# Optimization experiments

Measured on AMD Instinct MI355X. Metric: run time of the kernel, lower is better.

Reference implementation:

```python
import jax, jax.numpy as jnp
import numpy as np

D_MODEL = 1024
D_FF = 4096
BATCH = 4
SEQ = 2048
DECAY = 0.9
THRESH = 0.5


def setup_inputs() -> dict:
    key = jax.random.key(0)
    k1, k2, k3, k4 = jax.random.split(key, 4)
    spikes = jax.random.normal(k1, (BATCH, SEQ, D_MODEL), dtype=jnp.float32)
    # xavier-ish init scales matching gains 0.5/0.5/0.3 in the torch module
    s1 = 0.5 * np.sqrt(2.0 / (D_MODEL + D_FF))
    s2 = 0.5 * np.sqrt(2.0 / (D_MODEL + D_FF))
    sr = 0.3 * np.sqrt(2.0 / (D_MODEL + D_FF))
    W1 = jax.random.normal(k2, (D_FF, D_MODEL), dtype=jnp.float32) * s1
    W2 = jax.random.normal(k3, (D_MODEL, D_FF), dtype=jnp.float32) * s2
    Wr = jax.random.normal(k4, (D_FF, D_MODEL), dtype=jnp.float32) * sr
    return {"spikes": spikes, "W1": W1, "W2": W2, "Wr": Wr}


def reference(spikes, W1, W2, Wr):
    # spikes: [B, T, D]; W1, Wr: [F, D]; W2: [D, F]
    B, T, D = spikes.shape
    F = W1.shape[0]
    d = jnp.float32(DECAY)
    one_minus_d = jnp.float32(1.0 - DECAY)
    # Hoist time-independent projections out of the recurrence (same math as
    # the per-timestep nn.Linear calls in the torch loop).
    r_all = jax.nn.sigmoid(jnp.einsum('btd,fd->btf', spikes, Wr))  # [B,T,F]
    h_all = jnp.einsum('btd,fd->btf', spikes, W1)                   # [B,T,F]

    def step(carry, xs):
        act, rec = carry              # [B,F] each, init zeros (fresh buffers)
        r_t, h_t = xs                 # [B,F]
        rec = d * rec + one_minus_d * r_t                 # mixed receptance
        mixed = d * act + one_minus_d * h_t               # temporal state mix
        spike = (mixed > THRESH).astype(h_t.dtype)        # eval-mode spikes
        gated = spike * r_t
        # torch detaches current_activation each step
        return (jax.lax.stop_gradient(mixed), rec), gated

    init = (jnp.zeros((B, F), spikes.dtype), jnp.zeros((B, F), spikes.dtype))
    _, gated = jax.lax.scan(step,
                            init,
                            (jnp.swapaxes(r_all, 0, 1), jnp.swapaxes(h_all, 0, 1)))
    # gated: [T, B, F] -> output [B, T, D]
    out = jnp.einsum('tbf,df->btd', gated, W2)
    return out
```

## Files before the change

kernel.cpp:

```cpp
#include <hip/hip_runtime.h>
#include <math.h>

#define B_    4
#define T_    2048
#define D_    1024
#define F_    4096
#define R_    (B_*T_)
#define SEG_  64
#define L_    (T_/SEG_)
#define DECAYF 0.9f
#define OMDF   0.1f
#define FLAG_THRESH 0.45f

typedef __attribute__((ext_vector_type(4))) int   i32x4;
typedef __attribute__((ext_vector_type(8))) int   i32x8;
typedef __attribute__((ext_vector_type(4))) float f32x4;

__device__ __forceinline__ int pk_fp8x4(float x, float y, float z, float w) {
    int p = 0;
    p = __builtin_amdgcn_cvt_pk_fp8_f32(x, y, p, false);
    p = __builtin_amdgcn_cvt_pk_fp8_f32(z, w, p, true);
    return p;
}

__device__ __forceinline__ void gload_lds16(const void* g, void* l) {
    __builtin_amdgcn_global_load_lds(
        (const __attribute__((address_space(1))) unsigned int*)g,
        (__attribute__((address_space(3))) unsigned int*)l, 16, 0, 0);
}

#define KA_W1_BLOCKS  4096
#define KA_SEG_BLOCKS 256
#define KA_FLAG_BLOCKS 32

__global__ __launch_bounds__(256)
void kA_prologue(const float* __restrict__ spikes,
                 const float* __restrict__ W1,
                 unsigned char* __restrict__ w_f8,
                 float* __restrict__ seg_sum,
                 unsigned int* __restrict__ flags) {
    const int bid = blockIdx.x;
    const int tid = threadIdx.x;
    if (bid < KA_W1_BLOCKS) {
        int i = bid * 256 + tid;
        float4 v = ((const float4*)W1)[i];
        ((int*)w_f8)[i] = pk_fp8x4(8.f*v.x, 8.f*v.y, 8.f*v.z, 8.f*v.w);
    } else if (bid < KA_W1_BLOCKS + KA_SEG_BLOCKS) {
        int t = (bid - KA_W1_BLOCKS) * 256 + tid;
        int dg = t & (D_ / 4 - 1);
        int s = (t >> 8) & (SEG_ - 1);
        int b = t >> 14;
        const float4* sp4 = (const float4*)spikes;
        const int base = (b * T_ + s * L_) * (D_ / 4) + dg;
        float4 e = {0.f, 0.f, 0.f, 0.f};
#pragma unroll 8
        for (int k = 0; k < L_; ++k) {
            float4 x = sp4[base + k * (D_ / 4)];
            e.x = DECAYF * e.x + OMDF * x.x;
            e.y = DECAYF * e.y + OMDF * x.y;
            e.z = DECAYF * e.z + OMDF * x.z;
            e.w = DECAYF * e.w + OMDF * x.w;
        }
        ((float4*)seg_sum)[(b * SEG_ + s) * (D_ / 4) + dg] = e;
    } else {
        int i = (bid - KA_W1_BLOCKS - KA_SEG_BLOCKS) * 256 + tid;
        if (i < R_) flags[i] = 0u;
    }
}

__global__ __launch_bounds__(256)
void kB_seg_scan(const float* __restrict__ seg_sum,
                 float* __restrict__ start_state) {
    int g = blockIdx.x * 256 + threadIdx.x;
    int s = g & 63;
    int c = g >> 6;
    int d = c & (D_ - 1);
    int b = c >> 10;
    int idx = (b * SEG_ + s) * D_ + d;
    float v = seg_sum[idx];
    float wp = 0.0343368382f;
#pragma unroll
    for (int off = 1; off < SEG_; off <<= 1) {
        float u = __shfl_up(v, off, 64);
        if (s >= off) v += wp * u;
        wp *= wp;
    }
    float pv = __shfl_up(v, 1, 64);
    start_state[idx] = (s == 0) ? 0.f : pv;
}

__global__ __launch_bounds__(256)
void kC_ema_fp8(const float* __restrict__ spikes,
                const float* __restrict__ start_state,
                unsigned char* __restrict__ a_f8) {
    int t = blockIdx.x * 256 + threadIdx.x;
    int dg = t & (D_ / 4 - 1);
    int s = (t >> 8) & (SEG_ - 1);
    int b = t >> 14;
    const float4* sp4 = (const float4*)spikes;
    const int base = (b * T_ + s * L_) * (D_ / 4) + dg;
    float4 e = ((const float4*)start_state)[(b * SEG_ + s) * (D_ / 4) + dg];
#pragma unroll 8
    for (int k = 0; k < L_; ++k) {
        float4 x = sp4[base + k * (D_ / 4)];
        e.x = DECAYF * e.x + OMDF * x.x;
        e.y = DECAYF * e.y + OMDF * x.y;
        e.z = DECAYF * e.z + OMDF * x.z;
        e.w = DECAYF * e.w + OMDF * x.w;
        ((int*)a_f8)[base + k * (D_ / 4)] =
            pk_fp8x4(8.f*e.x, 8.f*e.y, 8.f*e.z, 8.f*e.w);
    }
}

__global__ __launch_bounds__(256)
void k2_mfma_flags(const unsigned char* __restrict__ A,
                   const unsigned char* __restrict__ Bw,
                   unsigned int* __restrict__ flags) {
    __shared__ __align__(16) unsigned char lA[128 * 128];
    __shared__ __align__(16) unsigned char lB[128 * 128];
    const int tid = threadIdx.x;
    const int w = tid >> 6;
    const int lane = tid & 63;
    const int m0 = blockIdx.y * 128;
    const int n0 = blockIdx.x * 128;
    const int wm = w >> 1, wn = w & 1;
    const int rown = lane & 15;
    const int kgrp = lane >> 4;
    const int c0 = 2 * kgrp;

    f32x4 acc[4][4] = {};

    for (int k0 = 0; k0 < D_; k0 += 128) {
        __syncthreads();
#pragma unroll
        for (int r = 0; r < 4; ++r) {
            const int Ibase = r * 256 + w * 64;
            const int I = Ibase + lane;
            const int row = I >> 3;
            const int cl = (I & 7) ^ (row & 7);
            gload_lds16(&A [(size_t)(m0 + row) * D_ + k0 + cl * 16], &lA[Ibase * 16]);
            gload_lds16(&Bw[(size_t)(n0 + row) * D_ + k0 + cl * 16], &lB[Ibase * 16]);
        }
        __syncthreads();

        i32x8 af[4], bf[4];
#pragma unroll
        for (int i = 0; i < 4; ++i) {
            const int ra = wm * 64 + i * 16 + rown;
            i32x4 lo = *(const i32x4*)&lA[ra * 128 + ((c0    ) ^ (ra & 7)) * 16];
            i32x4 hi = *(const i32x4*)&lA[ra * 128 + ((c0 + 1) ^ (ra & 7)) * 16];
            af[i] = (i32x8){lo.x, lo.y, lo.z, lo.w, hi.x, hi.y, hi.z, hi.w};
            const int rb = wn * 64 + i * 16 + rown;
            i32x4 lo2 = *(const i32x4*)&lB[rb * 128 + ((c0    ) ^ (rb & 7)) * 16];
            i32x4 hi2 = *(const i32x4*)&lB[rb * 128 + ((c0 + 1) ^ (rb & 7)) * 16];
            bf[i] = (i32x8){lo2.x, lo2.y, lo2.z, lo2.w, hi2.x, hi2.y, hi2.z, hi2.w};
        }
#pragma unroll
        for (int i = 0; i < 4; ++i)
#pragma unroll
            for (int j = 0; j < 4; ++j)
                acc[i][j] = __builtin_amdgcn_mfma_scale_f32_16x16x128_f8f6f4(
                    af[i], bf[j], acc[i][j],
                    0, 0,
                    0, 124,
                    0, 124);
    }

    const int quad = lane >> 4;
#pragma unroll
    for (int i = 0; i < 4; ++i) {
#pragma unroll
        for (int v = 0; v < 4; ++v) {
            float mx =     acc[i][0][v];
            mx = fmaxf(mx, acc[i][1][v]);
            mx = fmaxf(mx, acc[i][2][v]);
            mx = fmaxf(mx, acc[i][3][v]);
            if (mx > FLAG_THRESH)
                atomicOr(&flags[m0 + wm * 64 + i * 16 + quad * 4 + v], 1u);
        }
    }
}

__global__ __launch_bounds__(256)
void k4_output(const float* __restrict__ spikes,
               const float* __restrict__ start_state,
               const float* __restrict__ W1,
               const float* __restrict__ Wr,
               const float* __restrict__ W2,
               const unsigned int* __restrict__ flags,
               float* __restrict__ out) {
    const int row = blockIdx.x;
    const int tid = threadIdx.x;
    float4 o = {0.f, 0.f, 0.f, 0.f};

    if (flags[row] == 0u) {
        *(float4*)&out[(size_t)row * D_ + tid * 4] = o;
        return;
    }

    __shared__ float se[D_];
    __shared__ float sp[D_];
    __shared__ float red[256];
    __shared__ int nspk;
    __shared__ int spk_list[256];

    const int b = row / T_;
    const int t = row % T_;
    const int seg = t / L_;
    const int off = t % L_;
    const int segbase = (b * T_ + seg * L_) * D_;

    for (int i = tid; i < D_; i += 256) {
        float e = start_state[(b * SEG_ + seg) * D_ + i];
        for (int j = 0; j <= off; ++j)
            e = DECAYF * e + OMDF * spikes[segbase + j * D_ + i];
        se[i] = e;
        sp[i] = spikes[(size_t)row * D_ + i];
    }
    if (tid == 0) nspk = 0;
    __syncthreads();

    for (int f0 = 0; f0 < F_; f0 += 256) {
        int f = f0 + tid;
        float mix = 0.f;
        for (int k = 0; k < D_; ++k) mix += se[k] * W1[(size_t)f * D_ + k];
        if (mix > 0.5f) {
            int idx = atomicAdd(&nspk, 1);
            spk_list[idx] = f;
        }
        __syncthreads();
        int n = nspk;
        for (int i = 0; i < n; ++i) {
            int fs = spk_list[i];
            float part = 0.f;
#pragma unroll
            for (int k = 0; k < 4; ++k)
                part += sp[tid * 4 + k] * Wr[(size_t)fs * D_ + tid * 4 + k];
            red[tid] = part;
            __syncthreads();
            for (int sft = 128; sft > 0; sft >>= 1) {
                if (tid < sft) red[tid] += red[tid + sft];
                __syncthreads();
            }
            float r = 1.f / (1.f + expf(-red[0]));
            __syncthreads();
            o.x += r * W2[(size_t)(tid * 4 + 0) * F_ + fs];
            o.y += r * W2[(size_t)(tid * 4 + 1) * F_ + fs];
            o.z += r * W2[(size_t)(tid * 4 + 2) * F_ + fs];
            o.w += r * W2[(size_t)(tid * 4 + 3) * F_ + fs];
        }
        __syncthreads();
        if (tid == 0) nspk = 0;
        __syncthreads();
    }
    *(float4*)&out[(size_t)row * D_ + tid * 4] = o;
}

extern "C" void kernel_launch(void* const* d_in, const int* in_sizes, int n_in,
                              void* d_out, int out_size, void* d_ws, size_t ws_size,
                              hipStream_t stream) {
    const float* spikes = (const float*)d_in[0];
    const float* W1     = (const float*)d_in[1];
    const float* W2     = (const float*)d_in[2];
    const float* Wr     = (const float*)d_in[3];
    float* out = (float*)d_out;

    char* ws = (char*)d_ws;
    float* seg_sum      = (float*)ws;
    float* start_state  = seg_sum + (size_t)B_ * SEG_ * D_;
    unsigned int* flags = (unsigned int*)(start_state + (size_t)B_ * SEG_ * D_);
    unsigned char* a_f8 = (unsigned char*)(flags + R_);
    unsigned char* w_f8 = a_f8 + (size_t)R_ * D_;

    kA_prologue<<<KA_W1_BLOCKS + KA_SEG_BLOCKS + KA_FLAG_BLOCKS, 256, 0, stream>>>(
        spikes, W1, w_f8, seg_sum, flags);
    kB_seg_scan<<<(B_ * D_ * 64) / 256, 256, 0, stream>>>(seg_sum, start_state);
    kC_ema_fp8<<<(B_ * SEG_ * D_ / 4) / 256, 256, 0, stream>>>(spikes, start_state, a_f8);

    dim3 g2(F_ / 128, R_ / 128);
    k2_mfma_flags<<<g2, 256, 0, stream>>>(a_f8, w_f8, flags);

    k4_output<<<R_, 256, 0, stream>>>(spikes, start_state, W1, Wr, W2, flags, out);
}
```

Baseline: 203.8 us.

## Switch flag GEMM to 32x32x64 fp8 MFMA with smaller K tile

After: 379.6 us. 86.3% more time.

```diff
diff --git a/kernel.cpp b/kernel.cpp
--- a/kernel.cpp
+++ b/kernel.cpp
@@ -12,9 +12,9 @@
 #define OMDF   0.1f
 #define FLAG_THRESH 0.45f
 
-typedef __attribute__((ext_vector_type(4))) int   i32x4;
-typedef __attribute__((ext_vector_type(8))) int   i32x8;
-typedef __attribute__((ext_vector_type(4))) float f32x4;
+typedef __attribute__((ext_vector_type(4)))  int   i32x4;
+typedef __attribute__((ext_vector_type(8)))  int   i32x8;
+typedef __attribute__((ext_vector_type(16))) float f32x16;
 
 __device__ __forceinline__ int pk_fp8x4(float x, float y, float z, float w) {
     int p = 0;
@@ -112,71 +112,79 @@
     }
 }
 
-__global__ __launch_bounds__(256)
+__global__ __launch_bounds__(256, 3)
 void k2_mfma_flags(const unsigned char* __restrict__ A,
                    const unsigned char* __restrict__ Bw,
                    unsigned int* __restrict__ flags) {
-    __shared__ __align__(16) unsigned char lA[128 * 128];
-    __shared__ __align__(16) unsigned char lB[128 * 128];
+    __shared__ __align__(16) unsigned char lA[128 * 64];
+    __shared__ __align__(16) unsigned char lB[128 * 64];
     const int tid = threadIdx.x;
     const int w = tid >> 6;
     const int lane = tid & 63;
     const int m0 = blockIdx.y * 128;
     const int n0 = blockIdx.x * 128;
     const int wm = w >> 1, wn = w & 1;
-    const int rown = lane & 15;
-    const int kgrp = lane >> 4;
-    const int c0 = 2 * kgrp;
-
-    f32x4 acc[4][4] = {};
-
-    for (int k0 = 0; k0 < D_; k0 += 128) {
-        __syncthreads();
-#pragma unroll
-        for (int r = 0; r < 4; ++r) {
+    const int col = lane & 31;
+    const int kg  = lane >> 5;
+
+    int offA[2][2], offB[2][2];
+#pragma unroll
+    for (int i = 0; i < 2; ++i) {
+        const int ra = wm * 64 + i * 32 + col;
+        const int swa = (ra >> 1) & 3;
+        offA[i][0] = ra * 64 + ((2 * kg    ) ^ swa) * 16;
+        offA[i][1] = ra * 64 + ((2 * kg + 1) ^ swa) * 16;
+        const int rb = wn * 64 + i * 32 + col;
+        const int swb = (rb >> 1) & 3;
+        offB[i][0] = rb * 64 + ((2 * kg    ) ^ swb) * 16;
+        offB[i][1] = rb * 64 + ((2 * kg + 1) ^ swb) * 16;
+    }
+
+    f32x16 acc[2][2] = {};
+
+    for (int k0 = 0; k0 < D_; k0 += 64) {
+        __syncthreads();
+#pragma unroll
+        for (int r = 0; r < 2; ++r) {
             const int Ibase = r * 256 + w * 64;
             const int I = Ibase + lane;
-            const int row = I >> 3;
-            const int cl = (I & 7) ^ (row & 7);
-            gload_lds16(&A [(size_t)(m0 + row) * D_ + k0 + cl * 16], &lA[Ibase * 16]);
-            gload_lds16(&Bw[(size_t)(n0 + row) * D_ + k0 + cl * 16], &lB[Ibase * 16]);
-        }
-        __syncthreads();
-
-        i32x8 af[4], bf[4];
-#pragma unroll
-        for (int i = 0; i < 4; ++i) {
-            const int ra = wm * 64 + i * 16 + rown;
-            i32x4 lo = *(const i32x4*)&lA[ra * 128 + ((c0    ) ^ (ra & 7)) * 16];
-            i32x4 hi = *(const i32x4*)&lA[ra * 128 + ((c0 + 1) ^ (ra & 7)) * 16];
-            af[i] = (i32x8){lo.x, lo.y, lo.z, lo.w, hi.x, hi.y, hi.z, hi.w};
-            const int rb = wn * 64 + i * 16 + rown;
-            i32x4 lo2 = *(const i32x4*)&lB[rb * 128 + ((c0    ) ^ (rb & 7)) * 16];
-            i32x4 hi2 = *(const i32x4*)&lB[rb * 128 + ((c0 + 1) ^ (rb & 7)) * 16];
-            bf[i] = (i32x8){lo2.x, lo2.y, lo2.z, lo2.w, hi2.x, hi2.y, hi2.z, hi2.w};
-        }
-#pragma unroll
-        for (int i = 0; i < 4; ++i)
-#pragma unroll
-            for (int j = 0; j < 4; ++j)
-                acc[i][j] = __builtin_amdgcn_mfma_scale_f32_16x16x128_f8f6f4(
+            const int row = I >> 2;
+            const int lc = (I & 3) ^ ((row >> 1) & 3);
+            gload_lds16(&A [(size_t)(m0 + row) * D_ + k0 + lc * 16], &lA[Ibase * 16]);
+            gload_lds16(&Bw[(size_t)(n0 + row) * D_ + k0 + lc * 16], &lB[Ibase * 16]);
+        }
+        __syncthreads();
+
+        i32x8 af[2], bf[2];
+#pragma unroll
+        for (int i = 0; i < 2; ++i) {
+            i32x4 a0 = *(const i32x4*)&lA[offA[i][0]];
+            i32x4 a1 = *(const i32x4*)&lA[offA[i][1]];
+            af[i] = (i32x8){a0.x, a0.y, a0.z, a0.w, a1.x, a1.y, a1.z, a1.w};
+            i32x4 b0 = *(const i32x4*)&lB[offB[i][0]];
+            i32x4 b1 = *(const i32x4*)&lB[offB[i][1]];
+            bf[i] = (i32x8){b0.x, b0.y, b0.z, b0.w, b1.x, b1.y, b1.z, b1.w};
+        }
+#pragma unroll
+        for (int i = 0; i < 2; ++i)
+#pragma unroll
+            for (int j = 0; j < 2; ++j)
+                acc[i][j] = __builtin_amdgcn_mfma_scale_f32_32x32x64_f8f6f4(
                     af[i], bf[j], acc[i][j],
                     0, 0,
                     0, 124,
                     0, 124);
     }
 
-    const int quad = lane >> 4;
-#pragma unroll
-    for (int i = 0; i < 4; ++i) {
-#pragma unroll
-        for (int v = 0; v < 4; ++v) {
-            float mx =     acc[i][0][v];
-            mx = fmaxf(mx, acc[i][1][v]);
-            mx = fmaxf(mx, acc[i][2][v]);
-            mx = fmaxf(mx, acc[i][3][v]);
-            if (mx > FLAG_THRESH)
-                atomicOr(&flags[m0 + wm * 64 + i * 16 + quad * 4 + v], 1u);
+#pragma unroll
+    for (int i = 0; i < 2; ++i) {
+#pragma unroll
+        for (int reg = 0; reg < 16; ++reg) {
+            float mx = fmaxf(acc[i][0][reg], acc[i][1][reg]);
+            if (mx > FLAG_THRESH) {
+                const int rr = (reg & 3) + 8 * (reg >> 2) + 4 * kg;
+                atomicOr(&flags[m0 + wm * 64 + i * 32 + rr], 1u);
+            }
         }
     }
 }
```
